# Kernel optimization log

Hardware: AMD Instinct MI355X
Metric: run time of the kernel (lower is better)

The kernel has to match this reference:

```python
import jax, jax.numpy as jnp
import numpy as np

# Hyperparameters matching the torch module instantiation
STRIDE = (2, 2, 2)
PADDING = (1, 1, 1)
OUTPUT_PADDING = (1, 1, 1)
DILATION = (2, 2, 2)
KERNEL = (3, 3, 3)


def setup_inputs() -> dict:
    key = jax.random.key(0)
    k1, k2, k3 = jax.random.split(key, 3)
    x = jax.random.normal(k1, (2, 64, 32, 32, 32), dtype=jnp.float32)
    # torch ConvTranspose3d weight layout: (C_in, C_out//groups, kD, kH, kW)
    weight = jax.random.normal(k2, (64, 32, 3, 3, 3), dtype=jnp.float32) * 0.05
    bias = jax.random.normal(k3, (32,), dtype=jnp.float32) * 0.05
    return {"x": x, "weight": weight, "bias": bias}


def reference(x, weight, bias):
    # Same math as the naive torch module: zero-insertion upsample by stride,
    # symmetric pad by dilation*(k-1)-padding, dense conv3d with the spatially
    # flipped weight at rhs dilation, trailing output_padding, then bias add.
    # lhs_dilation performs the zero-insertion implicitly (identical result).
    pad = tuple(max(0, d * (k - 1) - p)
                for d, k, p in zip(DILATION, KERNEL, PADDING))
    # (C_in, C_out, k,k,k) -> (C_out, C_in, k,k,k), flipped spatially
    w = jnp.flip(jnp.transpose(weight, (1, 0, 2, 3, 4)), axis=(2, 3, 4))
    out = jax.lax.conv_general_dilated(
        x, w,
        window_strides=(1, 1, 1),
        padding=[(p, p) for p in pad],
        lhs_dilation=STRIDE,
        rhs_dilation=DILATION,
        dimension_numbers=("NCDHW", "OIDHW", "NCDHW"),
    )
    opd, oph, opw = OUTPUT_PADDING
    out = jnp.pad(out, ((0, 0), (0, 0), (0, opd), (0, oph), (0, opw)))
    return out + bias[None, :, None, None, None]
```

## Files before the change

kernel.cpp:

```cpp
#include <hip/hip_runtime.h>


#define DOUT 66
#define PL (DOUT*DOUT)

typedef _Float16 half8 __attribute__((ext_vector_type(8)));
typedef float    floatx16 __attribute__((ext_vector_type(16)));

#define X16_N_F16  2228224
#define ROW_B      4352
#define ZSLAB_OFF  112640
#define X16_OFF    131072

#define PB_W    216
#define PB_X    512
#define PB_B    579
#define PREP_GRID (PB_W + PB_X + PB_B)

__global__ void __launch_bounds__(256) prep(
    const float* __restrict__ x, const float* __restrict__ w,
    const float* __restrict__ bias, _Float16* __restrict__ wA,
    _Float16* __restrict__ x16, uint4* __restrict__ zslab,
    float* __restrict__ out)
{
    const int tid = threadIdx.x;
    unsigned b = blockIdx.x;

    if (b < PB_W) {
        int o = b * 256 + tid;
        int j = o & 7;
        int tmp = o >> 3;
        int lane = tmp & 63;
        int g = tmp >> 6;
        int cc = g / 27, tap = g - cc * 27;
        int co = lane & 31, khalf = lane >> 5;
        int ci = cc * 16 + khalf * 8 + j;
        wA[o] = (_Float16)w[ci * 864 + co * 27 + tap];
        return;
    }
    b -= PB_W;
    if (b < PB_X) {
        const int id = b & 31;
        const int q2 = (b >> 5) & 7;
        const int n  = b >> 8;
        const int iw = tid & 31;
        const int cihalf = (tid >> 5) & 1;
        const int ihq = tid >> 6;
        const int ih = q2 * 4 + ihq;

        if (b == 0) {
            zslab[2 * tid]     = make_uint4(0, 0, 0, 0);
            zslab[2 * tid + 1] = make_uint4(0, 0, 0, 0);
        }

        const float* xr = x + (size_t)n * 2097152 + (id * 32 + ih) * 32 + iw;
        _Float16* drow = x16 + (size_t)n * X16_N_F16 + (id * 32 + ih) * 2176;
        const int c0 = cihalf * 32;

        float f[32];
        #pragma unroll
        for (int j = 0; j < 32; ++j) f[j] = xr[(size_t)(c0 + j) * 32768];
        #pragma unroll
        for (int k = 0; k < 4; ++k) {
            unsigned pk[4];
            #pragma unroll
            for (int j = 0; j < 4; ++j)
                pk[j] = __builtin_bit_cast(unsigned,
                    __builtin_amdgcn_cvt_pkrtz(f[8 * k + 2 * j], f[8 * k + 2 * j + 1]));
            const int ccg = cihalf * 4 + k;
            *(uint4*)(drow + ccg * 272 + (iw + 1) * 8) =
                make_uint4(pk[0], pk[1], pk[2], pk[3]);
        }
        if (tid < 64) {
            const int ihq2 = tid >> 4;
            const int rem  = tid & 15;
            const int ccg  = rem >> 1, side = rem & 1;
            _Float16* hz = x16 + (size_t)n * X16_N_F16 +
                (id * 32 + q2 * 4 + ihq2) * 2176 + ccg * 272 + (side ? 264 : 0);
            *(uint4*)hz = make_uint4(0, 0, 0, 0);
        }
        return;
    }
    b -= PB_X;
    {
        const unsigned base = b * 4096u;
        #pragma unroll
        for (int j = 0; j < 16; ++j) {
            unsigned g = base + j * 256u + tid;
            if (g >= 2369952u) continue;
            unsigned pl = g / 1089u;
            unsigned slot = g - pl * 1089u;
            unsigned e  = pl % 34u;
            unsigned nc = pl / 34u;
            unsigned od = (e < 33u) ? 2u * e : 65u;
            float v = bias[nc & 31u];
            float4* p = (float4*)(out + ((size_t)nc * DOUT + od) * PL);
            p[slot] = make_float4(v, v, v, v);
        }
    }
}

__global__ void __launch_bounds__(256, 3) convt(
    const _Float16* __restrict__ x16, const _Float16* __restrict__ wA,
    const _Float16* __restrict__ zslab, const float* __restrict__ bias,
    float* __restrict__ out)
{
    __shared__ __align__(16) unsigned char xlds[52224];

    const int tid  = threadIdx.x;
    const int lane = tid & 63;
    const int wv   = tid >> 6;

    unsigned b = blockIdx.x;
    const unsigned xcd = b & 7u;
    const int n   = xcd & 1;
    const unsigned rest = b >> 3;
    const int dp  = rest & 31;
    const int hq2 = rest >> 5;
    const int hpg = (int)((xcd >> 1) * 4 + hq2);
    const int hpb = hpg * 2;

    const char* xby = (const char*)(x16 + (size_t)n * X16_N_F16);
    const char* zby = (const char*)zslab;
    for (int m = wv; m < 51; m += 4) {
        int c = m * 64 + lane;
        int r = c >> 8;
        r = c / 272;
        int q = c - r * 272;
        int idl = r >> 2, ihl = r & 3;
        int id = dp - 1 + idl, ih = hpb - 1 + ihl;
        bool v = ((unsigned)id < 32u) & ((unsigned)ih < 32u);
        const char* g = v ? (xby + (id * 32 + ih) * ROW_B + q * 16) : (zby + q * 16);
        __builtin_amdgcn_global_load_lds(
            (const __attribute__((address_space(1))) void*)g,
            (__attribute__((address_space(3))) void*)(xlds + m * 1024),
            16, 0, 0);
    }

    uint4 A[27];
    const _Float16* wl = wA + ((size_t)wv * 27 * 64 + lane) * 8;
    #pragma unroll
    for (int t = 0; t < 27; ++t) A[t] = *(const uint4*)(wl + t * 512);

    __syncthreads();

    const int wp    = lane & 31;
    const int khalf = lane >> 5;
    const int cbase = (2 * wv + khalf) * 544 + wp * 16;

    floatx16 acc0 = {}, acc1 = {};
    #pragma unroll
    for (int kd = 0; kd < 3; ++kd)
    #pragma unroll
    for (int kh = 0; kh < 3; ++kh)
    #pragma unroll
    for (int kw = 0; kw < 3; ++kw) {
        const int tap = (kd * 3 + kh) * 3 + kw;
        const int row0 = (2 - kd) * 4 + (2 - kh);
        const uint4* bp0 = (const uint4*)(xlds + row0 * ROW_B + cbase + (2 - kw) * 16);
        acc0 = __builtin_amdgcn_mfma_f32_32x32x16_f16(
            __builtin_bit_cast(half8, A[tap]),
            __builtin_bit_cast(half8, bp0[0]), acc0, 0, 0, 0);
        const uint4* bp1 = (const uint4*)((const char*)bp0 + ROW_B);
        acc1 = __builtin_amdgcn_mfma_f32_32x32x16_f16(
            __builtin_bit_cast(half8, A[tap]),
            __builtin_bit_cast(half8, bp1[0]), acc1, 0, 0, 0);
    }

    __syncthreads();
    float* part = (float*)xlds;
    if (wv != 0) {
        #pragma unroll
        for (int r = 0; r < 16; ++r)
            part[((wv * 2 + 0) * 16 + r) * 64 + lane] = acc0[r];
    }
    if (wv != 1) {
        #pragma unroll
        for (int r = 0; r < 16; ++r)
            part[((wv * 2 + 1) * 16 + r) * 64 + lane] = acc1[r];
    }
    __syncthreads();

    const int od = 2 * dp + 1;
    if (wv <= 1) {
        float s[16];
        #pragma unroll
        for (int r = 0; r < 16; ++r) {
            s[r] = (wv == 0) ? acc0[r] : acc1[r];
            #pragma unroll
            for (int w2 = 0; w2 < 4; ++w2) {
                if (w2 == wv) continue;
                s[r] += part[((w2 * 2 + wv) * 16 + r) * 64 + lane];
            }
        }
        const int oh = 2 * (hpb + wv) + 1;
        #pragma unroll
        for (int r = 0; r < 16; ++r) {
            const int co = (r & 3) + 8 * (r >> 2) + 4 * khalf;
            const float bv = bias[co];
            float2* orow = (float2*)(out +
                ((size_t)(n * 32 + co) * DOUT + od) * PL + oh * DOUT);
            orow[wp] = make_float2(bv, s[r] + bv);
            if (wp == 31) orow[32] = make_float2(bv, bv);
        }
    } else {
        const int oh = (wv == 2) ? 2 * hpb : 2 * hpb + 2;
        const int oht = (wv == 2) ? 64 : 65;
        const bool tails = (hpg == 15);
        #pragma unroll
        for (int r = 0; r < 16; ++r) {
            const int co = (r & 3) + 8 * (r >> 2) + 4 * khalf;
            const float bv = bias[co];
            float* pbase = out + ((size_t)(n * 32 + co) * DOUT + od) * PL;
            float2* erow = (float2*)(pbase + oh * DOUT);
            erow[wp] = make_float2(bv, bv);
            if (wp == 31) erow[32] = make_float2(bv, bv);
            if (tails) {
                float2* trow = (float2*)(pbase + oht * DOUT);
                trow[wp] = make_float2(bv, bv);
                if (wp == 31) trow[32] = make_float2(bv, bv);
            }
        }
    }
}

extern "C" void kernel_launch(void* const* d_in, const int* in_sizes, int n_in,
                              void* d_out, int out_size, void* d_ws, size_t ws_size,
                              hipStream_t stream) {
    const float* x    = (const float*)d_in[0];
    const float* wgt  = (const float*)d_in[1];
    const float* bias = (const float*)d_in[2];
    float* out = (float*)d_out;
    _Float16* wA    = (_Float16*)d_ws;
    uint4*    zslab = (uint4*)((char*)d_ws + ZSLAB_OFF);
    _Float16* x16   = (_Float16*)((char*)d_ws + X16_OFF);

    prep<<<PREP_GRID, 256, 0, stream>>>(x, wgt, bias, wA, x16, zslab, out);
    convt<<<1024, 256, 0, stream>>>(x16, wA, (const _Float16*)zslab, bias, out);
}
```

Before: 109.0 us.

## Fuse x fp16 conversion and bias-plane fill into conv kernel

Removes the separate prep pass that converted x to a padded fp16 layout in workspace. The conv kernel now reads fp32 x directly, converts it and writes the halo slab into LDS itself. It also writes the even-depth bias-only planes with nontemporal stores. This drops an extra global round trip of x and a large separate fill pass. In exchange each block reloads overlapping fp32 rows (about 3x reuse across neighbouring blocks) and does more strided global loads before the MFMA loop.

```diff
diff --git a/kernel.cpp b/kernel.cpp
--- a/kernel.cpp
+++ b/kernel.cpp
@@ -6,104 +6,27 @@
 
 typedef _Float16 half8 __attribute__((ext_vector_type(8)));
 typedef float    floatx16 __attribute__((ext_vector_type(16)));
+typedef float    floatx4  __attribute__((ext_vector_type(4)));
 
-#define X16_N_F16  2228224
-#define ROW_B      4352
-#define ZSLAB_OFF  112640
-#define X16_OFF    131072
+#define ROW_B 4352
 
-#define PB_W    216
-#define PB_X    512
-#define PB_B    579
-#define PREP_GRID (PB_W + PB_X + PB_B)
-
-__global__ void __launch_bounds__(256) prep(
-    const float* __restrict__ x, const float* __restrict__ w,
-    const float* __restrict__ bias, _Float16* __restrict__ wA,
-    _Float16* __restrict__ x16, uint4* __restrict__ zslab,
-    float* __restrict__ out)
-{
-    const int tid = threadIdx.x;
-    unsigned b = blockIdx.x;
-
-    if (b < PB_W) {
-        int o = b * 256 + tid;
-        int j = o & 7;
-        int tmp = o >> 3;
-        int lane = tmp & 63;
-        int g = tmp >> 6;
-        int cc = g / 27, tap = g - cc * 27;
-        int co = lane & 31, khalf = lane >> 5;
-        int ci = cc * 16 + khalf * 8 + j;
-        wA[o] = (_Float16)w[ci * 864 + co * 27 + tap];
-        return;
-    }
-    b -= PB_W;
-    if (b < PB_X) {
-        const int id = b & 31;
-        const int q2 = (b >> 5) & 7;
-        const int n  = b >> 8;
-        const int iw = tid & 31;
-        const int cihalf = (tid >> 5) & 1;
-        const int ihq = tid >> 6;
-        const int ih = q2 * 4 + ihq;
-
-        if (b == 0) {
-            zslab[2 * tid]     = make_uint4(0, 0, 0, 0);
-            zslab[2 * tid + 1] = make_uint4(0, 0, 0, 0);
-        }
-
-        const float* xr = x + (size_t)n * 2097152 + (id * 32 + ih) * 32 + iw;
-        _Float16* drow = x16 + (size_t)n * X16_N_F16 + (id * 32 + ih) * 2176;
-        const int c0 = cihalf * 32;
-
-        float f[32];
-        #pragma unroll
-        for (int j = 0; j < 32; ++j) f[j] = xr[(size_t)(c0 + j) * 32768];
-        #pragma unroll
-        for (int k = 0; k < 4; ++k) {
-            unsigned pk[4];
-            #pragma unroll
-            for (int j = 0; j < 4; ++j)
-                pk[j] = __builtin_bit_cast(unsigned,
-                    __builtin_amdgcn_cvt_pkrtz(f[8 * k + 2 * j], f[8 * k + 2 * j + 1]));
-            const int ccg = cihalf * 4 + k;
-            *(uint4*)(drow + ccg * 272 + (iw + 1) * 8) =
-                make_uint4(pk[0], pk[1], pk[2], pk[3]);
-        }
-        if (tid < 64) {
-            const int ihq2 = tid >> 4;
-            const int rem  = tid & 15;
-            const int ccg  = rem >> 1, side = rem & 1;
-            _Float16* hz = x16 + (size_t)n * X16_N_F16 +
-                (id * 32 + q2 * 4 + ihq2) * 2176 + ccg * 272 + (side ? 264 : 0);
-            *(uint4*)hz = make_uint4(0, 0, 0, 0);
-        }
-        return;
-    }
-    b -= PB_X;
-    {
-        const unsigned base = b * 4096u;
-        #pragma unroll
-        for (int j = 0; j < 16; ++j) {
-            unsigned g = base + j * 256u + tid;
-            if (g >= 2369952u) continue;
-            unsigned pl = g / 1089u;
-            unsigned slot = g - pl * 1089u;
-            unsigned e  = pl % 34u;
-            unsigned nc = pl / 34u;
-            unsigned od = (e < 33u) ? 2u * e : 65u;
-            float v = bias[nc & 31u];
-            float4* p = (float4*)(out + ((size_t)nc * DOUT + od) * PL);
-            p[slot] = make_float4(v, v, v, v);
-        }
-    }
+__global__ void __launch_bounds__(256) wprep(const float* __restrict__ w,
+                                             _Float16* __restrict__ wA) {
+    int o = blockIdx.x * 256 + threadIdx.x;
+    if (o >= 55296) return;
+    int j = o & 7;
+    int tmp = o >> 3;
+    int lane = tmp & 63;
+    int g = tmp >> 6;
+    int cc = g / 27, tap = g - cc * 27;
+    int co = lane & 31, khalf = lane >> 5;
+    int ci = cc * 16 + khalf * 8 + j;
+    wA[o] = (_Float16)w[ci * 864 + co * 27 + tap];
 }
 
 __global__ void __launch_bounds__(256, 3) convt(
-    const _Float16* __restrict__ x16, const _Float16* __restrict__ wA,
-    const _Float16* __restrict__ zslab, const float* __restrict__ bias,
-    float* __restrict__ out)
+    const float* __restrict__ x, const _Float16* __restrict__ wA,
+    const float* __restrict__ bias, float* __restrict__ out)
 {
     __shared__ __align__(16) unsigned char xlds[52224];
 
@@ -111,7 +34,7 @@
     const int lane = tid & 63;
     const int wv   = tid >> 6;
 
-    unsigned b = blockIdx.x;
+    const unsigned b = blockIdx.x;
     const unsigned xcd = b & 7u;
     const int n   = xcd & 1;
     const unsigned rest = b >> 3;
@@ -120,28 +43,41 @@
     const int hpg = (int)((xcd >> 1) * 4 + hq2);
     const int hpb = hpg * 2;
 
-    const char* xby = (const char*)(x16 + (size_t)n * X16_N_F16);
-    const char* zby = (const char*)zslab;
-    for (int m = wv; m < 51; m += 4) {
-        int c = m * 64 + lane;
-        int r = c >> 8;
-        r = c / 272;
-        int q = c - r * 272;
-        int idl = r >> 2, ihl = r & 3;
-        int id = dp - 1 + idl, ih = hpb - 1 + ihl;
-        bool v = ((unsigned)id < 32u) & ((unsigned)ih < 32u);
-        const char* g = v ? (xby + (id * 32 + ih) * ROW_B + q * 16) : (zby + q * 16);
-        __builtin_amdgcn_global_load_lds(
-            (const __attribute__((address_space(1))) void*)g,
-            (__attribute__((address_space(3))) void*)(xlds + m * 1024),
-            16, 0, 0);
-    }
-
     uint4 A[27];
     const _Float16* wl = wA + ((size_t)wv * 27 * 64 + lane) * 8;
     #pragma unroll
     for (int t = 0; t < 27; ++t) A[t] = *(const uint4*)(wl + t * 512);
 
+    {
+        const float* xg = x + (size_t)n * 2097152 + (size_t)(8 * (tid >> 5)) * 32768
+                          + (tid & 31);
+        const int iw = tid & 31;
+        const int G  = tid >> 5;
+        #pragma unroll
+        for (int r = 0; r < 12; ++r) {
+            const int idl = r >> 2, ihl = r & 3;
+            const int id = dp - 1 + idl, ih = hpb - 1 + ihl;
+            uint4 pk = make_uint4(0u, 0u, 0u, 0u);
+            if (((unsigned)id < 32u) & ((unsigned)ih < 32u)) {
+                const float* xr = xg + (id * 32 + ih) * 32;
+                float f[8];
+                #pragma unroll
+                for (int j = 0; j < 8; ++j) f[j] = xr[(size_t)j * 32768];
+                pk.x = __builtin_bit_cast(unsigned, __builtin_amdgcn_cvt_pkrtz(f[0], f[1]));
+                pk.y = __builtin_bit_cast(unsigned, __builtin_amdgcn_cvt_pkrtz(f[2], f[3]));
+                pk.z = __builtin_bit_cast(unsigned, __builtin_amdgcn_cvt_pkrtz(f[4], f[5]));
+                pk.w = __builtin_bit_cast(unsigned, __builtin_amdgcn_cvt_pkrtz(f[6], f[7]));
+            }
+            *(uint4*)&xlds[r * ROW_B + G * 544 + (iw + 1) * 16] = pk;
+        }
+        if (tid < 192) {
+            const int row = tid >> 4;
+            const int rem = tid & 15;
+            const int ccg = rem >> 1, side = rem & 1;
+            *(uint4*)&xlds[row * ROW_B + ccg * 544 + (side ? 33 : 0) * 16] =
+                make_uint4(0u, 0u, 0u, 0u);
+        }
+    }
     __syncthreads();
 
     const int wp    = lane & 31;
@@ -222,6 +158,24 @@
             }
         }
     }
+
+    #pragma unroll
+    for (int k = 0; k < 3; ++k) {
+        unsigned p;
+        if (k == 0)      p = b;
+        else if (k == 1) p = b + 1024u;
+        else { if (b >= 128u) break; p = 2048u + b; }
+        const unsigned nc = p / 34u, e = p - nc * 34u;
+        const unsigned odp = (e < 33u) ? 2u * e : 65u;
+        const float v = bias[nc & 31u];
+        const floatx4 v4 = {v, v, v, v};
+        floatx4* pb = (floatx4*)(out + ((size_t)nc * DOUT + odp) * PL);
+        #pragma unroll
+        for (int j = 0; j < 5; ++j) {
+            const unsigned idx = j * 256u + tid;
+            if (idx < 1089u) __builtin_nontemporal_store(v4, pb + idx);
+        }
+    }
 }
 
 extern "C" void kernel_launch(void* const* d_in, const int* in_sizes, int n_in,
@@ -231,10 +185,8 @@
     const float* wgt  = (const float*)d_in[1];
     const float* bias = (const float*)d_in[2];
     float* out = (float*)d_out;
-    _Float16* wA    = (_Float16*)d_ws;
-    uint4*    zslab = (uint4*)((char*)d_ws + ZSLAB_OFF);
-    _Float16* x16   = (_Float16*)((char*)d_ws + X16_OFF);
+    _Float16* wA = (_Float16*)d_ws;
 
-    prep<<<PREP_GRID, 256, 0, stream>>>(x, wgt, bias, wA, x16, zslab, out);
-    convt<<<1024, 256, 0, stream>>>(x16, wA, (const _Float16*)zslab, bias, out);
+    wprep<<<216, 256, 0, stream>>>(wgt, wA);
+    convt<<<1024, 256, 0, stream>>>(x, wA, bias, out);
 }
```

Result: no change. 110.9 us (+1.8%).
